# Kernel optimization log

Hardware: AMD Instinct MI355X
Metric: run time of the kernel (lower is better)

Reference implementation:

```python
import jax, jax.numpy as jnp
import numpy as np

N_NODES = 100000
FEAT = 256
HID = 256
BATCH = 512
NUM_SAMPLES = [25, 10]  # layer_infos[0].num_samples, layer_infos[1].num_samples


def setup_inputs() -> dict:
    key = jax.random.key(0)
    ks = jax.random.split(key, 7)
    scale = 0.05
    return {
        "features": jax.random.normal(ks[0], (N_NODES, FEAT), dtype=jnp.float32),
        "adj": jax.random.randint(ks[1], (N_NODES, NUM_SAMPLES[0]), 0, N_NODES, dtype=jnp.int32),
        "batch": jax.random.randint(ks[2], (BATCH,), 0, N_NODES, dtype=jnp.int32),
        "W_self_0": jax.random.normal(ks[3], (FEAT, HID), dtype=jnp.float32) * scale,
        "W_neigh_0": jax.random.normal(ks[4], (FEAT, HID), dtype=jnp.float32) * scale,
        "W_self_1": jax.random.normal(ks[5], (HID, HID), dtype=jnp.float32) * scale,
        "W_neigh_1": jax.random.normal(ks[6], (HID, HID), dtype=jnp.float32) * scale,
    }


def reference(features, adj, batch, W_self_0, W_neigh_0, W_self_1, W_neigh_1):
    B = batch.shape[0]
    n_layers = 2
    # --- sample(): reverse-order neighbor expansion (deterministic: first-k slots) ---
    # hop 1 uses layer_infos[-1].num_samples = 10, hop 2 uses layer_infos[0].num_samples = 25
    s1 = adj[batch][:, : NUM_SAMPLES[1]].reshape(-1)  # [B*10]
    s2 = adj[s1][:, : NUM_SAMPLES[0]].reshape(-1)     # [B*250]
    support = [1, NUM_SAMPLES[1], NUM_SAMPLES[1] * NUM_SAMPLES[0]]  # [1, 10, 250]
    # --- gather input features per hop (irregular gather, memory bound) ---
    hidden = [features[batch], features[s1], features[s2]]
    Ws = [(W_self_0, W_neigh_0), (W_self_1, W_neigh_1)]
    for layer in range(n_layers):
        act = jax.nn.relu if layer < n_layers - 1 else (lambda x: x)
        W_s, W_n = Ws[layer]
        next_hidden = []
        for hop in range(n_layers - layer):
            n_smp = NUM_SAMPLES[n_layers - hop - 1]
            self_vecs = hidden[hop]  # [B*support[hop], d]
            neigh = hidden[hop + 1].reshape(B * support[hop], n_smp, -1)
            neigh_mean = neigh.mean(axis=1)  # mean aggregator
            # concat=False -> sum of self and neighbor transforms
            next_hidden.append(act(self_vecs @ W_s + neigh_mean @ W_n))
        hidden = next_hidden
    out = hidden[0]  # [B, HID]
    # GraphSAGE l2-normalizes final embeddings
    norm = jnp.maximum(jnp.linalg.norm(out, axis=1, keepdims=True), 1e-12)
    return out / norm
```

## Files before the change

kernel.cpp:

```cpp
#include <hip/hip_runtime.h>
#include <cstdint>
#include <cstddef>

#define NNODES 100000
#define FEATD  256
#define HIDD   256
#define NBATCH 512
#define FAN1   10
#define FAN2   25
#define NS1    (NBATCH*FAN1)
#define MTOT   (NBATCH+NS1)

typedef __attribute__((ext_vector_type(8))) short short8;
typedef __attribute__((ext_vector_type(4))) float f32x4;

__device__ __forceinline__ unsigned short f2bf(float f) {
    unsigned int u = __float_as_uint(f);
    unsigned int r = (u + 0x7fffu + ((u >> 16) & 1u)) >> 16;
    return (unsigned short)r;
}

__global__ __launch_bounds__(256) void k_wcvt(
    const float* __restrict__ Ws0, const float* __restrict__ Wn0,
    unsigned short* __restrict__ B0t) {
    int i4 = (blockIdx.x * 256 + threadIdx.x) * 4;
    const float* W = (i4 < 65536) ? Ws0 : Wn0;
    int base = i4 & 65535;
    int kl   = base >> 8;
    int n    = base & 255;
    int k    = (i4 < 65536) ? kl : (kl + 256);
    float4 v = *reinterpret_cast<const float4*>(W + base);
    B0t[(size_t)(n + 0) * 512 + k] = f2bf(v.x);
    B0t[(size_t)(n + 1) * 512 + k] = f2bf(v.y);
    B0t[(size_t)(n + 2) * 512 + k] = f2bf(v.z);
    B0t[(size_t)(n + 3) * 512 + k] = f2bf(v.w);
}

__global__ __launch_bounds__(256) void k_nmean_pack(
    const float* __restrict__ feat, const int* __restrict__ adj,
    const int* __restrict__ batch, unsigned short* __restrict__ A0) {
    const int w    = blockIdx.x * 4 + (threadIdx.x >> 6);
    const int lane = threadIdx.x & 63;

    int node;
    if (w < NBATCH) {
        node = batch[w];
    } else {
        int i = w - NBATCH;
        int b = i / FAN1;
        int j = i - b * FAN1;
        node = adj[(size_t)batch[b] * FAN2 + j];
    }
    const float* selfp = feat + (size_t)node * FEATD + lane * 4;
    float4 selfv = *reinterpret_cast<const float4*>(selfp);

    const int* arow = adj + (size_t)node * FAN2;
    int myidx = (lane < FAN2) ? arow[lane] : 0;

    float4 acc = make_float4(0.f, 0.f, 0.f, 0.f);
    if (w < NBATCH) {
        #pragma unroll
        for (int k = 0; k < FAN1; ++k) {
            int nb = __shfl(myidx, k);
            float4 v = *reinterpret_cast<const float4*>(
                feat + (size_t)nb * FEATD + lane * 4);
            acc.x += v.x; acc.y += v.y; acc.z += v.z; acc.w += v.w;
        }
        const float s = 1.0f / (float)FAN1;
        acc.x *= s; acc.y *= s; acc.z *= s; acc.w *= s;
    } else {
        #pragma unroll
        for (int k = 0; k < FAN2; ++k) {
            int nb = __shfl(myidx, k);
            float4 v = *reinterpret_cast<const float4*>(
                feat + (size_t)nb * FEATD + lane * 4);
            acc.x += v.x; acc.y += v.y; acc.z += v.z; acc.w += v.w;
        }
        const float s = 1.0f / (float)FAN2;
        acc.x *= s; acc.y *= s; acc.z *= s; acc.w *= s;
    }

    ushort4 ps, pn;
    ps.x = f2bf(selfv.x); ps.y = f2bf(selfv.y);
    ps.z = f2bf(selfv.z); ps.w = f2bf(selfv.w);
    pn.x = f2bf(acc.x);   pn.y = f2bf(acc.y);
    pn.z = f2bf(acc.z);   pn.w = f2bf(acc.w);
    unsigned short* dst = A0 + (size_t)w * 512;
    *reinterpret_cast<ushort4*>(dst + lane * 4)       = ps;
    *reinterpret_cast<ushort4*>(dst + 256 + lane * 4) = pn;
}

__global__ __launch_bounds__(256) void k_gemm0(
    const unsigned short* __restrict__ A0, const unsigned short* __restrict__ B0t,
    float* __restrict__ H0, float* __restrict__ H1) {
    __shared__ __align__(16) unsigned short As[64][72];
    __shared__ __align__(16) unsigned short Bs[64][72];
    const int t   = threadIdx.x;
    const int wv  = t >> 6;
    const int l   = t & 63;
    const int q   = l >> 4;
    const int m15 = l & 15;
    const int rt  = blockIdx.x >> 2;
    const int ct  = blockIdx.x & 3;
    const int r0  = rt * 64, c0 = ct * 64;

    f32x4 acc[4];
    #pragma unroll
    for (int f = 0; f < 4; ++f) acc[f] = (f32x4)0.f;

    for (int kt = 0; kt < 8; ++kt) {
        const int k0 = kt * 64;
        #pragma unroll
        for (int i = 0; i < 2; ++i) {
            int s = t + i * 256;
            int row = s >> 3, k8 = (s & 7) * 8;
            *reinterpret_cast<short8*>(&As[row][k8]) =
                *reinterpret_cast<const short8*>(
                    A0 + (size_t)(r0 + row) * 512 + k0 + k8);
        }
        #pragma unroll
        for (int i = 0; i < 2; ++i) {
            int s = t + i * 256;
            int nl = s >> 3, k8 = (s & 7) * 8;
            *reinterpret_cast<short8*>(&Bs[nl][k8]) =
                *reinterpret_cast<const short8*>(
                    B0t + (size_t)(c0 + nl) * 512 + k0 + k8);
        }
        __syncthreads();
        #pragma unroll
        for (int s = 0; s < 2; ++s) {
            const int kk = q * 8 + s * 32;
            short8 a = *reinterpret_cast<const short8*>(&As[wv * 16 + m15][kk]);
            #pragma unroll
            for (int f = 0; f < 4; ++f) {
                short8 b = *reinterpret_cast<const short8*>(&Bs[f * 16 + m15][kk]);
                acc[f] = __builtin_amdgcn_mfma_f32_16x16x32_bf16(a, b, acc[f], 0, 0, 0);
            }
        }
        __syncthreads();
    }

    #pragma unroll
    for (int f = 0; f < 4; ++f) {
        const int n = c0 + f * 16 + m15;
        #pragma unroll
        for (int j = 0; j < 4; ++j) {
            int m = r0 + wv * 16 + q * 4 + j;
            float v = fmaxf(acc[f][j], 0.f);
            if (m < NBATCH)
                H0[(size_t)m * HIDD + n] = v;
            else
                H1[(size_t)(m - NBATCH) * HIDD + n] = v;
        }
    }
}

__global__ __launch_bounds__(256) void k_layer1(
    const float* __restrict__ H0, const float* __restrict__ H1,
    const float* __restrict__ Ws, const float* __restrict__ Wn,
    float* __restrict__ out) {
    __shared__ float At[4][512];
    const int t  = threadIdx.x;
    const int rb = blockIdx.x * 4;

    {
        int r = t >> 6, c4 = t & 63;
        *reinterpret_cast<float4*>(&At[r][c4 * 4]) =
            *reinterpret_cast<const float4*>(H0 + (size_t)(rb + r) * HIDD + c4 * 4);
    }
    {
        int r = t >> 6, c4 = t & 63;
        const float* base = H1 + (size_t)(rb + r) * FAN1 * HIDD + c4 * 4;
        float4 acc = make_float4(0.f, 0.f, 0.f, 0.f);
        #pragma unroll
        for (int j = 0; j < FAN1; ++j) {
            float4 v = *reinterpret_cast<const float4*>(base + (size_t)j * HIDD);
            acc.x += v.x; acc.y += v.y; acc.z += v.z; acc.w += v.w;
        }
        const float s = 1.0f / (float)FAN1;
        acc.x *= s; acc.y *= s; acc.z *= s; acc.w *= s;
        *reinterpret_cast<float4*>(&At[r][256 + c4 * 4]) = acc;
    }
    __syncthreads();

    const int wv = t >> 6;
    const int tc = (t & 63) * 4;
    float4 acc = make_float4(0.f, 0.f, 0.f, 0.f);

    const float* Wh[2] = {Ws, Wn};
    #pragma unroll
    for (int half = 0; half < 2; ++half) {
        const float* W  = Wh[half] + tc;
        const int    ko = half * 256;
        for (int k4 = 0; k4 < 64; ++k4) {
            int k = k4 * 4;
            float4 a = *reinterpret_cast<const float4*>(&At[wv][ko + k]);
            const float* ap = &a.x;
            #pragma unroll
            for (int kk = 0; kk < 4; ++kk) {
                float4 w = *reinterpret_cast<const float4*>(W + (size_t)(k + kk) * HIDD);
                float av = ap[kk];
                acc.x += av * w.x; acc.y += av * w.y;
                acc.z += av * w.z; acc.w += av * w.w;
            }
        }
    }

    float p = acc.x*acc.x + acc.y*acc.y + acc.z*acc.z + acc.w*acc.w;
    #pragma unroll
    for (int off = 32; off >= 1; off >>= 1) p += __shfl_xor(p, off);
    float inv = 1.0f / fmaxf(sqrtf(p), 1e-12f);
    acc.x *= inv; acc.y *= inv; acc.z *= inv; acc.w *= inv;
    *reinterpret_cast<float4*>(out + (size_t)(rb + wv) * HIDD + tc) = acc;
}

extern "C" void kernel_launch(void* const* d_in, const int* in_sizes, int n_in,
                              void* d_out, int out_size, void* d_ws, size_t ws_size,
                              hipStream_t stream) {
    const float* feat  = (const float*)d_in[0];
    const int*   adj   = (const int*)d_in[1];
    const int*   batch = (const int*)d_in[2];
    const float* Ws0   = (const float*)d_in[3];
    const float* Wn0   = (const float*)d_in[4];
    const float* Ws1   = (const float*)d_in[5];
    const float* Wn1   = (const float*)d_in[6];
    float* out = (float*)d_out;

    char* ws = (char*)d_ws;
    unsigned short* A0  = (unsigned short*)(ws + 0);
    unsigned short* B0t = (unsigned short*)(ws + 5767168);
    float*          H0  = (float*)(ws + 6029312);
    float*          H1  = (float*)(ws + 6553600);

    k_wcvt<<<128, 256, 0, stream>>>(Ws0, Wn0, B0t);
    k_nmean_pack<<<MTOT / 4, 256, 0, stream>>>(feat, adj, batch, A0);
    k_gemm0<<<(MTOT / 64) * 4, 256, 0, stream>>>(A0, B0t, H0, H1);
    k_layer1<<<NBATCH / 4, 256, 0, stream>>>(H0, H1, Ws1, Wn1, out);
}
```

Baseline: 209.2 us.

## Fuse neighbor-mean gather into layer-0 GEMM and tile weight transpose through LDS

The separate gather/pack kernel and layer-0 GEMM are merged: each block gathers 16 rows (self plus neighbor mean, converted to bf16) straight into shared memory, then multiplies them against all 256 output columns. This removes the global A0 round trip and one kernel launch. The weight conversion kernel now transposes through an LDS tile so its global writes are coalesced, and the layer-1 kernel uses smaller blocks so there are more of them. The cost is that every block reloads the full B matrix, and the gather latency is no longer overlapped across separate kernels, and each block now has fewer rows to spread that latency over.

```diff
diff --git a/kernel.cpp b/kernel.cpp
--- a/kernel.cpp
+++ b/kernel.cpp
@@ -23,117 +23,109 @@
 __global__ __launch_bounds__(256) void k_wcvt(
     const float* __restrict__ Ws0, const float* __restrict__ Wn0,
     unsigned short* __restrict__ B0t) {
-    int i4 = (blockIdx.x * 256 + threadIdx.x) * 4;
-    const float* W = (i4 < 65536) ? Ws0 : Wn0;
-    int base = i4 & 65535;
-    int kl   = base >> 8;
-    int n    = base & 255;
-    int k    = (i4 < 65536) ? kl : (kl + 256);
-    float4 v = *reinterpret_cast<const float4*>(W + base);
-    B0t[(size_t)(n + 0) * 512 + k] = f2bf(v.x);
-    B0t[(size_t)(n + 1) * 512 + k] = f2bf(v.y);
-    B0t[(size_t)(n + 2) * 512 + k] = f2bf(v.z);
-    B0t[(size_t)(n + 3) * 512 + k] = f2bf(v.w);
-}
-
-__global__ __launch_bounds__(256) void k_nmean_pack(
+    __shared__ unsigned short Ts[64][72];
+    const int t  = threadIdx.x;
+    const int kt = blockIdx.x >> 2;
+    const int nt = blockIdx.x & 3;
+    const int k0 = kt * 64, n0 = nt * 64;
+    const float* W = (k0 < 256) ? (Ws0 + (size_t)k0 * 256)
+                                : (Wn0 + (size_t)(k0 - 256) * 256);
+    #pragma unroll
+    for (int i = 0; i < 4; ++i) {
+        int s  = t + i * 256;
+        int kr = s >> 4;
+        int c4 = s & 15;
+        float4 v = *reinterpret_cast<const float4*>(W + (size_t)kr * 256 + n0 + c4 * 4);
+        Ts[c4 * 4 + 0][kr] = f2bf(v.x);
+        Ts[c4 * 4 + 1][kr] = f2bf(v.y);
+        Ts[c4 * 4 + 2][kr] = f2bf(v.z);
+        Ts[c4 * 4 + 3][kr] = f2bf(v.w);
+    }
+    __syncthreads();
+    #pragma unroll
+    for (int i = 0; i < 2; ++i) {
+        int s  = t + i * 256;
+        int nl = s >> 3;
+        int k8 = (s & 7) * 8;
+        *reinterpret_cast<short8*>(B0t + (size_t)(n0 + nl) * 512 + k0 + k8) =
+            *reinterpret_cast<const short8*>(&Ts[nl][k8]);
+    }
+}
+
+__global__ __launch_bounds__(256) void k_gg0(
     const float* __restrict__ feat, const int* __restrict__ adj,
-    const int* __restrict__ batch, unsigned short* __restrict__ A0) {
-    const int w    = blockIdx.x * 4 + (threadIdx.x >> 6);
-    const int lane = threadIdx.x & 63;
-
-    int node;
-    if (w < NBATCH) {
-        node = batch[w];
-    } else {
-        int i = w - NBATCH;
-        int b = i / FAN1;
-        int j = i - b * FAN1;
-        node = adj[(size_t)batch[b] * FAN2 + j];
-    }
-    const float* selfp = feat + (size_t)node * FEATD + lane * 4;
-    float4 selfv = *reinterpret_cast<const float4*>(selfp);
-
-    const int* arow = adj + (size_t)node * FAN2;
-    int myidx = (lane < FAN2) ? arow[lane] : 0;
-
-    float4 acc = make_float4(0.f, 0.f, 0.f, 0.f);
-    if (w < NBATCH) {
-        #pragma unroll
-        for (int k = 0; k < FAN1; ++k) {
-            int nb = __shfl(myidx, k);
-            float4 v = *reinterpret_cast<const float4*>(
-                feat + (size_t)nb * FEATD + lane * 4);
-            acc.x += v.x; acc.y += v.y; acc.z += v.z; acc.w += v.w;
-        }
-        const float s = 1.0f / (float)FAN1;
-        acc.x *= s; acc.y *= s; acc.z *= s; acc.w *= s;
-    } else {
-        #pragma unroll
-        for (int k = 0; k < FAN2; ++k) {
-            int nb = __shfl(myidx, k);
-            float4 v = *reinterpret_cast<const float4*>(
-                feat + (size_t)nb * FEATD + lane * 4);
-            acc.x += v.x; acc.y += v.y; acc.z += v.z; acc.w += v.w;
-        }
-        const float s = 1.0f / (float)FAN2;
-        acc.x *= s; acc.y *= s; acc.z *= s; acc.w *= s;
-    }
-
-    ushort4 ps, pn;
-    ps.x = f2bf(selfv.x); ps.y = f2bf(selfv.y);
-    ps.z = f2bf(selfv.z); ps.w = f2bf(selfv.w);
-    pn.x = f2bf(acc.x);   pn.y = f2bf(acc.y);
-    pn.z = f2bf(acc.z);   pn.w = f2bf(acc.w);
-    unsigned short* dst = A0 + (size_t)w * 512;
-    *reinterpret_cast<ushort4*>(dst + lane * 4)       = ps;
-    *reinterpret_cast<ushort4*>(dst + 256 + lane * 4) = pn;
-}
-
-__global__ __launch_bounds__(256) void k_gemm0(
-    const unsigned short* __restrict__ A0, const unsigned short* __restrict__ B0t,
+    const int* __restrict__ batch, const unsigned short* __restrict__ B0t,
     float* __restrict__ H0, float* __restrict__ H1) {
-    __shared__ __align__(16) unsigned short As[64][72];
-    __shared__ __align__(16) unsigned short Bs[64][72];
+    __shared__ __align__(16) unsigned short As[16][520];
+    __shared__ __align__(16) unsigned short Bs[256][72];
     const int t   = threadIdx.x;
     const int wv  = t >> 6;
     const int l   = t & 63;
     const int q   = l >> 4;
     const int m15 = l & 15;
-    const int rt  = blockIdx.x >> 2;
-    const int ct  = blockIdx.x & 3;
-    const int r0  = rt * 64, c0 = ct * 64;
+    const int r0  = blockIdx.x * 16;
+    const bool isBatch = (r0 < NBATCH);
+    const int fan = isBatch ? FAN1 : FAN2;
+
+    for (int i = 0; i < 4; ++i) {
+        const int r = wv * 4 + i;
+        const int R = r0 + r;
+        int node;
+        if (isBatch) {
+            node = batch[R];
+        } else {
+            int idx = R - NBATCH;
+            int b   = idx / FAN1;
+            int j   = idx - b * FAN1;
+            node = adj[(size_t)batch[b] * FAN2 + j];
+        }
+        float4 selfv = *reinterpret_cast<const float4*>(
+            feat + (size_t)node * FEATD + l * 4);
+        const int* arow = adj + (size_t)node * FAN2;
+        int myidx = (l < FAN2) ? arow[l] : 0;
+        float4 acc = make_float4(0.f, 0.f, 0.f, 0.f);
+        for (int k = 0; k < fan; ++k) {
+            int nb = __shfl(myidx, k);
+            float4 v = *reinterpret_cast<const float4*>(
+                feat + (size_t)nb * FEATD + l * 4);
+            acc.x += v.x; acc.y += v.y; acc.z += v.z; acc.w += v.w;
+        }
+        const float s = 1.0f / (float)fan;
+        acc.x *= s; acc.y *= s; acc.z *= s; acc.w *= s;
+        ushort4 ps, pn;
+        ps.x = f2bf(selfv.x); ps.y = f2bf(selfv.y);
+        ps.z = f2bf(selfv.z); ps.w = f2bf(selfv.w);
+        pn.x = f2bf(acc.x);   pn.y = f2bf(acc.y);
+        pn.z = f2bf(acc.z);   pn.w = f2bf(acc.w);
+        *reinterpret_cast<ushort4*>(&As[r][l * 4])       = ps;
+        *reinterpret_cast<ushort4*>(&As[r][256 + l * 4]) = pn;
+    }
+    __syncthreads();
 
     f32x4 acc[4];
     #pragma unroll
     for (int f = 0; f < 4; ++f) acc[f] = (f32x4)0.f;
 
     for (int kt = 0; kt < 8; ++kt) {
-        const int k0 = kt * 64;
-        #pragma unroll
-        for (int i = 0; i < 2; ++i) {
-            int s = t + i * 256;
-            int row = s >> 3, k8 = (s & 7) * 8;
-            *reinterpret_cast<short8*>(&As[row][k8]) =
-                *reinterpret_cast<const short8*>(
-                    A0 + (size_t)(r0 + row) * 512 + k0 + k8);
-        }
-        #pragma unroll
-        for (int i = 0; i < 2; ++i) {
-            int s = t + i * 256;
-            int nl = s >> 3, k8 = (s & 7) * 8;
+        const int kb = kt * 64;
+        #pragma unroll
+        for (int i = 0; i < 8; ++i) {
+            int s  = t + i * 256;
+            int nl = s >> 3;
+            int k8 = (s & 7) * 8;
             *reinterpret_cast<short8*>(&Bs[nl][k8]) =
                 *reinterpret_cast<const short8*>(
-                    B0t + (size_t)(c0 + nl) * 512 + k0 + k8);
+                    B0t + (size_t)nl * 512 + kb + k8);
         }
         __syncthreads();
         #pragma unroll
-        for (int s = 0; s < 2; ++s) {
-            const int kk = q * 8 + s * 32;
-            short8 a = *reinterpret_cast<const short8*>(&As[wv * 16 + m15][kk]);
+        for (int s2 = 0; s2 < 2; ++s2) {
+            const int kk = s2 * 32 + q * 8;
+            short8 a = *reinterpret_cast<const short8*>(&As[m15][kb + kk]);
             #pragma unroll
             for (int f = 0; f < 4; ++f) {
-                short8 b = *reinterpret_cast<const short8*>(&Bs[f * 16 + m15][kk]);
+                short8 b = *reinterpret_cast<const short8*>(
+                    &Bs[wv * 64 + f * 16 + m15][kk]);
                 acc[f] = __builtin_amdgcn_mfma_f32_16x16x32_bf16(a, b, acc[f], 0, 0, 0);
             }
         }
@@ -142,12 +134,12 @@
 
     #pragma unroll
     for (int f = 0; f < 4; ++f) {
-        const int n = c0 + f * 16 + m15;
+        const int n = wv * 64 + f * 16 + m15;
         #pragma unroll
         for (int j = 0; j < 4; ++j) {
-            int m = r0 + wv * 16 + q * 4 + j;
+            int m = r0 + q * 4 + j;
             float v = fmaxf(acc[f][j], 0.f);
-            if (m < NBATCH)
+            if (isBatch)
                 H0[(size_t)m * HIDD + n] = v;
             else
                 H1[(size_t)(m - NBATCH) * HIDD + n] = v;
@@ -155,13 +147,13 @@
     }
 }
 
-__global__ __launch_bounds__(256) void k_layer1(
+__global__ __launch_bounds__(128) void k_layer1(
     const float* __restrict__ H0, const float* __restrict__ H1,
     const float* __restrict__ Ws, const float* __restrict__ Wn,
     float* __restrict__ out) {
-    __shared__ float At[4][512];
+    __shared__ float At[2][512];
     const int t  = threadIdx.x;
-    const int rb = blockIdx.x * 4;
+    const int rb = blockIdx.x * 2;
 
     {
         int r = t >> 6, c4 = t & 63;
@@ -227,13 +219,11 @@
     float* out = (float*)d_out;
 
     char* ws = (char*)d_ws;
-    unsigned short* A0  = (unsigned short*)(ws + 0);
-    unsigned short* B0t = (unsigned short*)(ws + 5767168);
-    float*          H0  = (float*)(ws + 6029312);
-    float*          H1  = (float*)(ws + 6553600);
-
-    k_wcvt<<<128, 256, 0, stream>>>(Ws0, Wn0, B0t);
-    k_nmean_pack<<<MTOT / 4, 256, 0, stream>>>(feat, adj, batch, A0);
-    k_gemm0<<<(MTOT / 64) * 4, 256, 0, stream>>>(A0, B0t, H0, H1);
-    k_layer1<<<NBATCH / 4, 256, 0, stream>>>(H0, H1, Ws1, Wn1, out);
-}
+    unsigned short* B0t = (unsigned short*)(ws + 0);
+    float*          H0  = (float*)(ws + 262144);
+    float*          H1  = (float*)(ws + 786432);
+
+    k_wcvt<<<32, 256, 0, stream>>>(Ws0, Wn0, B0t);
+    k_gg0<<<MTOT / 16, 256, 0, stream>>>(feat, adj, batch, B0t, H0, H1);
+    k_layer1<<<NBATCH / 2, 128, 0, stream>>>(H0, H1, Ws1, Wn1, out);
+}
```

After: 238.8 us. +14.1%, slower.
